# Optimization experiments

Hardware: AMD Instinct MI355X
Metric: run time of the kernel (lower is better)

Reference implementation:

```python
import jax, jax.numpy as jnp
import numpy as np

B, N, D = 4, 2048, 512
H, DH = 8, 64
MLP = 2048
EPS = 1e-5


def setup_inputs() -> dict:
    key = jax.random.key(0)
    ks = jax.random.split(key, 8)
    s = lambda fan_in: 1.0 / np.sqrt(fan_in)
    return {
        "x": jax.random.normal(ks[0], (B, N, D), jnp.float32),
        "ln1_g": jnp.ones((D,), jnp.float32),
        "ln1_b": jnp.zeros((D,), jnp.float32),
        "Wqkv": jax.random.normal(ks[1], (D, 3 * H * DH), jnp.float32) * s(D),
        "temperature": jnp.asarray(np.log(DH ** -0.5), jnp.float32),
        "Wo": jax.random.normal(ks[2], (H * DH, D), jnp.float32) * s(H * DH),
        "bo": jnp.zeros((D,), jnp.float32),
        "ln2_g": jnp.ones((D,), jnp.float32),
        "ln2_b": jnp.zeros((D,), jnp.float32),
        "W1": jax.random.normal(ks[3], (D, MLP), jnp.float32) * s(D),
        "b1": jnp.zeros((MLP,), jnp.float32),
        "W2": jax.random.normal(ks[4], (MLP, D), jnp.float32) * s(MLP),
        "b2": jnp.zeros((D,), jnp.float32),
    }


def _layernorm(x, g, b):
    mu = jnp.mean(x, axis=-1, keepdims=True)
    var = jnp.var(x, axis=-1, keepdims=True)
    return (x - mu) * jax.lax.rsqrt(var + EPS) * g + b


def _lsa(x, Wqkv, temperature, Wo, bo):
    b, n, _ = x.shape
    qkv = x @ Wqkv  # [b, n, 3*H*DH]
    q, k, v = jnp.split(qkv, 3, axis=-1)
    rs = lambda t: t.reshape(b, n, H, DH).transpose(0, 2, 1, 3)  # b h n d
    q, k, v = rs(q), rs(k), rs(v)
    dots = jnp.einsum("bhnd,bhmd->bhnm", q, k) * jnp.exp(temperature)
    mask_value = -jnp.finfo(dots.dtype).max
    eye = jnp.eye(n, dtype=bool)
    dots = jnp.where(eye, mask_value, dots)  # mask diagonal (LSA)
    attn = jax.nn.softmax(dots, axis=-1)
    out = jnp.einsum("bhnm,bhmd->bhnd", attn, v)
    out = out.transpose(0, 2, 1, 3).reshape(b, n, H * DH)
    return out @ Wo + bo


def _ffn(x, W1, b1, W2, b2):
    h = jax.nn.gelu(x @ W1 + b1, approximate=False)
    return h @ W2 + b2


def reference(x, ln1_g, ln1_b, Wqkv, temperature, Wo, bo,
              ln2_g, ln2_b, W1, b1, W2, b2):
    y = _lsa(_layernorm(x, ln1_g, ln1_b), Wqkv, temperature, Wo, bo) + x
    z = _ffn(_layernorm(y, ln2_g, ln2_b), W1, b1, W2, b2) + y
    return (z, x)
```

## Files before the change

kernel.cpp:

```cpp
#include <hip/hip_runtime.h>
#include <math.h>

typedef __attribute__((ext_vector_type(4))) float f32x4;
typedef __attribute__((ext_vector_type(8))) short short8;

#define DEV __device__ __forceinline__

DEV short f2bf(float f){
  union { float f; unsigned u; } v; v.f = f;
  unsigned r = v.u + 0x7fffu + ((v.u >> 16) & 1u);
  return (short)(r >> 16);
}
DEV float bf2f(short s){
  union { unsigned u; float f; } v; v.u = ((unsigned)(unsigned short)s) << 16; return v.f;
}
DEV float exp2_hw(float x){ float r; asm("v_exp_f32 %0, %1" : "=v"(r) : "v"(x)); return r; }
DEV float rcp_hw(float x){ float r; asm("v_rcp_f32 %0, %1" : "=v"(r) : "v"(x)); return r; }
DEV unsigned cvtpk(float a, float b){
  unsigned r; asm("v_cvt_pk_bf16_f32 %0, %1, %2" : "=v"(r) : "v"(a), "v"(b)); return r;
}
DEV void gload_lds16(const short* src, short* lds){
  __builtin_amdgcn_global_load_lds(
      (const __attribute__((address_space(1))) void*)src,
      (__attribute__((address_space(3))) void*)lds, 16, 0, 0);
}
DEV float gelu_fast(float v){
  float u = v * (0.79788456f + 0.03567741f * v * v);
  float e = exp2_hw(u * 2.88539008f);
  float th = 1.0f - 2.0f * rcp_hw(e + 1.0f);
  return 0.5f * v * (1.0f + th);
}

__global__ __launch_bounds__(256) void transpose_all_kernel(
    const float* __restrict__ Wqkv, short* __restrict__ wqkv_t,
    const float* __restrict__ Wo,   short* __restrict__ wo_t,
    const float* __restrict__ W1,   short* __restrict__ w1_t,
    const float* __restrict__ W2,   short* __restrict__ w2_t)
{
  int bid = blockIdx.x;
  const float* W; short* Wt; int K, N, nbx, local;
  if (bid < 768)       { W = Wqkv; Wt = wqkv_t; K = 512;  N = 1536; nbx = 48; local = bid; }
  else if (bid < 1024) { W = Wo;   Wt = wo_t;   K = 512;  N = 512;  nbx = 16; local = bid - 768; }
  else if (bid < 2048) { W = W1;   Wt = w1_t;   K = 512;  N = 2048; nbx = 64; local = bid - 1024; }
  else                 { W = W2;   Wt = w2_t;   K = 2048; N = 512;  nbx = 16; local = bid - 2048; }
  __shared__ float tile[32][33];
  int nb = (local % nbx) * 32, kb = (local / nbx) * 32;
  int tx = threadIdx.x & 31, ty = threadIdx.x >> 5;
  #pragma unroll
  for (int i = ty; i < 32; i += 8)
    tile[i][tx] = W[(size_t)(kb + i) * N + nb + tx];
  __syncthreads();
  #pragma unroll
  for (int i = ty; i < 32; i += 8)
    Wt[(size_t)(nb + i) * K + kb + tx] = f2bf(tile[tx][i]);
}

template<int COPYX>
__global__ __launch_bounds__(256) void ln_kernel(
    const float* __restrict__ x, const float* __restrict__ g,
    const float* __restrict__ b, short* __restrict__ out,
    float* __restrict__ xcopy)
{
  int row  = blockIdx.x * 4 + (threadIdx.x >> 6);
  int lane = threadIdx.x & 63;
  const float* xr = x + (size_t)row * 512 + lane * 8;
  f32x4 v0 = *(const f32x4*)(xr);
  f32x4 v1 = *(const f32x4*)(xr + 4);
  float s  = (v0[0]+v0[1]+v0[2]+v0[3]) + (v1[0]+v1[1]+v1[2]+v1[3]);
  float sq = (v0[0]*v0[0]+v0[1]*v0[1]+v0[2]*v0[2]+v0[3]*v0[3])
           + (v1[0]*v1[0]+v1[1]*v1[1]+v1[2]*v1[2]+v1[3]*v1[3]);
  #pragma unroll
  for (int off = 1; off < 64; off <<= 1) {
    s  += __shfl_xor(s, off);
    sq += __shfl_xor(sq, off);
  }
  float mu  = s * (1.0f / 512.0f);
  float var = sq * (1.0f / 512.0f) - mu * mu;
  float rstd = rsqrtf(var + 1e-5f);
  f32x4 g0 = *(const f32x4*)(g + lane * 8);
  f32x4 g1 = *(const f32x4*)(g + lane * 8 + 4);
  f32x4 b0 = *(const f32x4*)(b + lane * 8);
  f32x4 b1 = *(const f32x4*)(b + lane * 8 + 4);
  float o[8];
  #pragma unroll
  for (int j = 0; j < 4; ++j) o[j]     = (v0[j] - mu) * rstd * g0[j] + b0[j];
  #pragma unroll
  for (int j = 0; j < 4; ++j) o[4 + j] = (v1[j] - mu) * rstd * g1[j] + b1[j];
  uint4 pk;
  pk.x = cvtpk(o[0], o[1]); pk.y = cvtpk(o[2], o[3]);
  pk.z = cvtpk(o[4], o[5]); pk.w = cvtpk(o[6], o[7]);
  *(uint4*)(out + (size_t)row * 512 + lane * 8) = pk;
  if (COPYX) {
    float* xc = xcopy + (size_t)row * 512 + lane * 8;
    *(f32x4*)(xc)     = v0;
    *(f32x4*)(xc + 4) = v1;
  }
}

__global__ __launch_bounds__(256) void ln_bf_kernel(
    const short* __restrict__ x, const float* __restrict__ g,
    const float* __restrict__ b, short* __restrict__ out)
{
  int row  = blockIdx.x * 4 + (threadIdx.x >> 6);
  int lane = threadIdx.x & 63;
  short8 raw = *(const short8*)(x + (size_t)row * 512 + lane * 8);
  float v[8];
  #pragma unroll
  for (int j = 0; j < 8; ++j) v[j] = bf2f(raw[j]);
  float s = 0.f, sq = 0.f;
  #pragma unroll
  for (int j = 0; j < 8; ++j) { s += v[j]; sq += v[j] * v[j]; }
  #pragma unroll
  for (int off = 1; off < 64; off <<= 1) {
    s  += __shfl_xor(s, off);
    sq += __shfl_xor(sq, off);
  }
  float mu  = s * (1.0f / 512.0f);
  float var = sq * (1.0f / 512.0f) - mu * mu;
  float rstd = rsqrtf(var + 1e-5f);
  f32x4 g0 = *(const f32x4*)(g + lane * 8);
  f32x4 g1 = *(const f32x4*)(g + lane * 8 + 4);
  f32x4 b0 = *(const f32x4*)(b + lane * 8);
  f32x4 b1 = *(const f32x4*)(b + lane * 8 + 4);
  float o[8];
  #pragma unroll
  for (int j = 0; j < 4; ++j) o[j]     = (v[j] - mu) * rstd * g0[j] + b0[j];
  #pragma unroll
  for (int j = 0; j < 4; ++j) o[4 + j] = (v[4+j] - mu) * rstd * g1[j] + b1[j];
  uint4 pk;
  pk.x = cvtpk(o[0], o[1]); pk.y = cvtpk(o[2], o[3]);
  pk.z = cvtpk(o[4], o[5]); pk.w = cvtpk(o[6], o[7]);
  *(uint4*)(out + (size_t)row * 512 + lane * 8) = pk;
}

template<int EPI, int BM, typename OutT>
__global__ __launch_bounds__(256) void gemm_bt_kernel(
    const short* __restrict__ A, const short* __restrict__ Bt,
    OutT* __restrict__ C, const float* __restrict__ bias,
    const float* __restrict__ resid, const short* __restrict__ residb,
    int M, int N, int K)
{
  constexpr int MFR = BM / 32;
  constexpr int NFR = 4;
  constexpr int AI  = BM / 64;
  constexpr int BUF = BM * 32 + 128 * 32;
  __shared__ __align__(16) short smem[3 * BUF];

  int tid = threadIdx.x;
  int lane = tid & 63, wid = tid >> 6;
  int l16 = lane & 15, lq = lane >> 4;

  int gx = gridDim.x;
  int nwg = gx * gridDim.y;
  int orig = blockIdx.y * gx + blockIdx.x;
  int swz = (orig & 7) * (nwg >> 3) + (orig >> 3);
  int bn = swz % gx, bm = swz / gx;

  int wm = wid >> 1, wn = wid & 1;

  const short* gaP[AI];
  const short* gbP[2];
  #pragma unroll
  for (int i = 0; i < AI; ++i) {
    int gg = i * 4 + wid;
    gaP[i] = A + (size_t)(bm * BM + gg * 16 + l16) * K + lq * 8;
  }
  #pragma unroll
  for (int i = 0; i < 2; ++i) {
    int gg = i * 4 + wid;
    gbP[i] = Bt + (size_t)(bn * 128 + gg * 16 + l16) * K + lq * 8;
  }

  auto STAGE = [&](int bufi, int k0) {
    short* base = smem + bufi * BUF;
    #pragma unroll
    for (int i = 0; i < AI; ++i)
      gload_lds16(gaP[i] + k0, base + (i * 4 + wid) * 512);
    #pragma unroll
    for (int i = 0; i < 2; ++i)
      gload_lds16(gbP[i] + k0, base + BM * 32 + (i * 4 + wid) * 512);
  };

  f32x4 acc[MFR][NFR] = {};

  STAGE(0, 0);
  STAGE(1, 32);

  int nt = K >> 5;
  for (int t = 0; t < nt; ++t) {
    if (t + 1 < nt) {
      if constexpr (AI == 2) asm volatile("s_waitcnt vmcnt(4)" ::: "memory");
      else                   asm volatile("s_waitcnt vmcnt(3)" ::: "memory");
    } else {
      asm volatile("s_waitcnt vmcnt(0)" ::: "memory");
    }
    __builtin_amdgcn_s_barrier();
    __builtin_amdgcn_sched_barrier(0);
    if (t + 2 < nt) STAGE((t + 2) % 3, (t + 2) << 5);

    const short* base = smem + (t % 3) * BUF;
    short8 af[MFR], bfr[NFR];
    #pragma unroll
    for (int m = 0; m < MFR; ++m)
      af[m] = *(const short8*)(base + (wm * MFR + m) * 512 + lane * 8);
    #pragma unroll
    for (int n = 0; n < NFR; ++n)
      bfr[n] = *(const short8*)(base + BM * 32 + (wn * NFR + n) * 512 + lane * 8);
    __builtin_amdgcn_s_setprio(1);
    #pragma unroll
    for (int m = 0; m < MFR; ++m)
      #pragma unroll
      for (int n = 0; n < NFR; ++n)
        acc[m][n] = __builtin_amdgcn_mfma_f32_16x16x32_bf16(af[m], bfr[n], acc[m][n], 0, 0, 0);
    __builtin_amdgcn_s_setprio(0);
  }

  float bv[NFR];
  #pragma unroll
  for (int n = 0; n < NFR; ++n)
    bv[n] = bias[bn * 128 + (wn * NFR + n) * 16 + l16];

  #pragma unroll
  for (int m = 0; m < MFR; ++m) {
    #pragma unroll
    for (int r = 0; r < 4; ++r) {
      int row = bm * BM + (wm * MFR + m) * 16 + lq * 4 + r;
      #pragma unroll
      for (int n = 0; n < NFR; ++n) {
        int col = bn * 128 + (wn * NFR + n) * 16 + l16;
        float v = acc[m][n][r] + bv[n];
        if (EPI == 4) v += resid[(size_t)row * N + col];
        if (EPI == 5) v += bf2f(residb[(size_t)row * N + col]);
        if constexpr (sizeof(OutT) == 2)
          ((short*)C)[(size_t)row * N + col] = f2bf(v);
        else
          ((float*)C)[(size_t)row * N + col] = v;
      }
    }
  }
}

template<int EPI>
__global__ __launch_bounds__(512) void gemm256_kernel(
    const short* __restrict__ A, const short* __restrict__ Bt,
    short* __restrict__ C, const float* __restrict__ bias,
    short* __restrict__ vt, int M, int N, int K)
{
  constexpr int BUF = 24576;
  __shared__ __align__(16) short smem[3 * BUF];

  int tid = threadIdx.x;
  int lane = tid & 63, wid = tid >> 6;
  int l16 = lane & 15, lq = lane >> 4;

  int gx = gridDim.x;
  int nwg = gx * gridDim.y;
  int orig = blockIdx.y * gx + blockIdx.x;
  int swz = (orig & 7) * (nwg >> 3) + (orig >> 3);
  int bn = swz % gx, bm = swz / gx;

  int wm = wid >> 1, wn = wid & 1;

  const short* gaP[4];
  const short* gbP[2];
  #pragma unroll
  for (int i = 0; i < 4; ++i) {
    int g = i * 8 + wid;
    gaP[i] = A + (size_t)(bm * 256 + (g >> 1) * 16 + l16) * K + (g & 1) * 32 + lq * 8;
  }
  #pragma unroll
  for (int i = 0; i < 2; ++i) {
    int g = i * 8 + wid;
    gbP[i] = Bt + (size_t)(bn * 128 + (g >> 1) * 16 + l16) * K + (g & 1) * 32 + lq * 8;
  }

  auto STAGE = [&](int bufi, int k0) {
    short* base = smem + bufi * BUF;
    #pragma unroll
    for (int i = 0; i < 4; ++i)
      gload_lds16(gaP[i] + k0, base + (i * 8 + wid) * 512);
    #pragma unroll
    for (int i = 0; i < 2; ++i)
      gload_lds16(gbP[i] + k0, base + 16384 + (i * 8 + wid) * 512);
  };

  f32x4 acc[4][4] = {};

  STAGE(0, 0);
  STAGE(1, 64);

  int nt = K >> 6;
  for (int t = 0; t < nt; ++t) {
    if (t + 1 < nt) asm volatile("s_waitcnt vmcnt(6)" ::: "memory");
    else            asm volatile("s_waitcnt vmcnt(0)" ::: "memory");
    __builtin_amdgcn_s_barrier();
    __builtin_amdgcn_sched_barrier(0);
    if (t + 2 < nt) STAGE((t + 2) % 3, (t + 2) << 6);

    const short* base = smem + (t % 3) * BUF;
    #pragma unroll
    for (int kc = 0; kc < 2; ++kc) {
      short8 af[4], bfr[4];
      #pragma unroll
      for (int m = 0; m < 4; ++m)
        af[m] = *(const short8*)(base + ((wm * 4 + m) * 2 + kc) * 512 + lane * 8);
      #pragma unroll
      for (int n = 0; n < 4; ++n)
        bfr[n] = *(const short8*)(base + 16384 + ((wn * 4 + n) * 2 + kc) * 512 + lane * 8);
      __builtin_amdgcn_s_setprio(1);
      #pragma unroll
      for (int m = 0; m < 4; ++m)
        #pragma unroll
        for (int n = 0; n < 4; ++n)
          acc[m][n] = __builtin_amdgcn_mfma_f32_16x16x32_bf16(af[m], bfr[n], acc[m][n], 0, 0, 0);
      __builtin_amdgcn_s_setprio(0);
    }
  }

  if (EPI == 3 && bn >= 8) {
    __syncthreads();
    short* T = smem;
    #pragma unroll
    for (int m = 0; m < 4; ++m)
      #pragma unroll
      for (int n = 0; n < 4; ++n) {
        int c = wn * 64 + n * 16 + l16;
        #pragma unroll
        for (int r = 0; r < 4; ++r) {
          int rowl = wm * 64 + m * 16 + lq * 4 + r;
          T[c * 256 + (rowl ^ ((c & 7) << 4))] = f2bf(acc[m][n][r]);
        }
      }
    __syncthreads();
    int b2 = bm >> 3;
    int nnb = (bm & 7) * 256;
    int tn = tid & 31, cw = tid >> 5;
    #pragma unroll
    for (int c8 = 0; c8 < 8; ++c8) {
      int c = c8 * 16 + cw;
      short8 v = *(const short8*)(T + c * 256 + ((tn * 8) ^ ((c & 7) << 4)));
      if (tn & 1) {
        short8 w;
        #pragma unroll
        for (int j = 0; j < 8; ++j) w[j] = v[j ^ 4];
        v = w;
      }
      int c2 = bn * 128 + c - 1024;
      int bh = b2 * 8 + (c2 >> 6);
      int d  = c2 & 63;
      *(short8*)(vt + ((size_t)(bh * 64 + d)) * 2048 + nnb + tn * 8) = v;
    }
    return;
  }

  #pragma unroll
  for (int m = 0; m < 4; ++m) {
    #pragma unroll
    for (int r = 0; r < 4; ++r) {
      int row = bm * 256 + (wm * 4 + m) * 16 + lq * 4 + r;
      #pragma unroll
      for (int n = 0; n < 4; ++n) {
        int col = bn * 128 + (wn * 4 + n) * 16 + l16;
        C[(size_t)row * N + col] = f2bf(acc[m][n][r]);
      }
    }
  }
}

__global__ __launch_bounds__(512, 2) void gemm8p_kernel(
    const short* __restrict__ A, const short* __restrict__ Bt,
    short* __restrict__ C, const float* __restrict__ bias,
    int M, int N, int K)
{
  __shared__ __align__(16) short smem[2 * 32768];

  int tid = threadIdx.x;
  int lane = tid & 63, wid = tid >> 6;
  int l16 = lane & 15, lq = lane >> 4;
  int wm = wid >> 2, wn = wid & 3;

  int gx = gridDim.x;
  int nwg = gx * gridDim.y;
  int orig = blockIdx.y * gx + blockIdx.x;
  int swz = (orig & 7) * (nwg >> 3) + (orig >> 3);
  int bn = swz % gx, bm = swz / gx;

  const short* gaP[4];
  const short* gbP[4];
  #pragma unroll
  for (int i = 0; i < 4; ++i) {
    int idx = i * 512 + tid;
    int g = idx >> 6, ln = idx & 63;
    gaP[i] = A  + (size_t)(bm * 256 + (g >> 1) * 16 + (ln & 15)) * K
                + (g & 1) * 32 + (ln >> 4) * 8;
    gbP[i] = Bt + (size_t)(bn * 256 + (g >> 1) * 16 + (ln & 15)) * K
                + (g & 1) * 32 + (ln >> 4) * 8;
  }

  auto STAGE_A = [&](int buf, int k0) {
    short* dst = smem + buf * 32768;
    #pragma unroll
    for (int i = 0; i < 4; ++i)
      gload_lds16(gaP[i] + k0, dst + ((size_t)(i * 512 + tid)) * 8);
  };
  auto STAGE_B_LO = [&](int buf, int k0) {
    short* dst = smem + buf * 32768 + 16384;
    #pragma unroll
    for (int i = 0; i < 2; ++i)
      gload_lds16(gbP[i] + k0, dst + ((size_t)(i * 512 + tid)) * 8);
  };
  auto STAGE_B_HI = [&](int buf, int k0) {
    short* dst = smem + buf * 32768 + 16384;
    #pragma unroll
    for (int i = 2; i < 4; ++i)
      gload_lds16(gbP[i] + k0, dst + ((size_t)(i * 512 + tid)) * 8);
  };

  f32x4 acc[8][4] = {};

  STAGE_A(0, 0);
  STAGE_B_LO(0, 0); STAGE_B_HI(0, 0);
  STAGE_B_LO(1, 64); STAGE_B_HI(1, 64);
  asm volatile("s_waitcnt vmcnt(4)" ::: "memory");
  __builtin_amdgcn_s_barrier();

  int nt = K >> 6;
  for (int t = 0; t < nt; ++t) {
    int cur = t & 1;
    const short* As_ = smem + cur * 32768;
    const short* Bs_ = As_ + 16384;
    short8 bf[4][2];

    #pragma unroll
    for (int p = 0; p < 4; ++p) {
      short8 af[2][2];
      #pragma unroll
      for (int mm = 0; mm < 2; ++mm)
        #pragma unroll
        for (int kc = 0; kc < 2; ++kc)
          af[mm][kc] = *(const short8*)(As_ + ((wm * 8 + 2 * p + mm) * 2 + kc) * 512 + lane * 8);
      if (p == 0) {
        #pragma unroll
        for (int n = 0; n < 4; ++n)
          #pragma unroll
          for (int kc = 0; kc < 2; ++kc)
            bf[n][kc] = *(const short8*)(Bs_ + ((wn * 4 + n) * 2 + kc) * 512 + lane * 8);
      }
      if (p == 0 && t + 1 < nt) STAGE_A(cur ^ 1, (t + 1) << 6);
      if (p == 1 && t + 2 < nt) STAGE_B_LO(cur, (t + 2) << 6);
      if (p == 2 && t + 2 < nt) STAGE_B_HI(cur, (t + 2) << 6);

      __builtin_amdgcn_s_barrier();
      asm volatile("s_waitcnt lgkmcnt(0)" ::: "memory");
      __builtin_amdgcn_sched_barrier(0);
      __builtin_amdgcn_s_setprio(1);
      #pragma unroll
      for (int mm = 0; mm < 2; ++mm)
        #pragma unroll
        for (int n = 0; n < 4; ++n)
          #pragma unroll
          for (int kc = 0; kc < 2; ++kc)
            acc[2 * p + mm][n] = __builtin_amdgcn_mfma_f32_16x16x32_bf16(
                af[mm][kc], bf[n][kc], acc[2 * p + mm][n], 0, 0, 0);
      __builtin_amdgcn_s_setprio(0);
      if (p < 3) {
        __builtin_amdgcn_s_barrier();
      } else {
        if (t + 2 < nt) asm volatile("s_waitcnt vmcnt(4)" ::: "memory");
        else            asm volatile("s_waitcnt vmcnt(0)" ::: "memory");
        __builtin_amdgcn_s_barrier();
      }
    }
  }

  float bv[4];
  #pragma unroll
  for (int n = 0; n < 4; ++n)
    bv[n] = bias[bn * 256 + (wn * 4 + n) * 16 + l16];
  #pragma unroll
  for (int m = 0; m < 8; ++m) {
    #pragma unroll
    for (int r = 0; r < 4; ++r) {
      int row = bm * 256 + wm * 128 + m * 16 + lq * 4 + r;
      #pragma unroll
      for (int n = 0; n < 4; ++n) {
        int col = bn * 256 + (wn * 4 + n) * 16 + l16;
        C[(size_t)row * N + col] = f2bf(gelu_fast(acc[m][n][r] + bv[n]));
      }
    }
  }
}

__global__ __launch_bounds__(512, 4) void attn_kernel(
    const short* __restrict__ qkv, const short* __restrict__ vt,
    const float* __restrict__ temp_ptr,
    short* __restrict__ Op0, short* __restrict__ Op1, float* __restrict__ Lbuf)
{
  __shared__ __align__(16) short smem[16384];

  int tid = threadIdx.x;
  int lane = tid & 63, wid = tid >> 6;
  int l16 = lane & 15, lq = lane >> 4;
  int hi = lq >> 1, lq0 = lq & 1;

  int orig = blockIdx.y * 8 + blockIdx.x;
  int swz = (orig & 7) * 64 + (orig >> 3);
  int qb = swz & 7;
  int rr = swz >> 3;
  int bh = rr & 31, slice = rr >> 5;
  int b = bh >> 3, h = bh & 7;

  const short* qbase = qkv + (size_t)b * 2048 * 1536 + h * 64;
  const short* kbase = qbase + 512;
  const short* vbase = vt + (size_t)bh * 64 * 2048;
  int kslice = slice * 1024;

  float scale = __expf(temp_ptr[0]) * 1.44269504f;
  int q0 = qb * 256 + wid * 32;

  short8 qfrag[2][2];
  #pragma unroll
  for (int qf = 0; qf < 2; ++qf) {
    int qrow = q0 + qf * 16 + l16;
    #pragma unroll
    for (int c = 0; c < 2; ++c) {
      short8 raw = *(const short8*)(qbase + (size_t)qrow * 1536 + c * 32 + lq * 8);
      short8 sc;
      #pragma unroll
      for (int j = 0; j < 8; ++j) sc[j] = f2bf(bf2f(raw[j]) * scale);
      qfrag[qf][c] = sc;
    }
  }

  f32x4 accO[2][4] = {};
  float l[2] = {0.f, 0.f};

  auto STAGE = [&](int bufi, int k0) {
    int sub = wid >> 1, cc = wid & 1;
    const short* srcK = kbase + (size_t)(k0 + sub * 16 + l16) * 1536 + cc * 32 + lq * 8;
    gload_lds16(srcK, smem + bufi * 4096 + wid * 512);
    const short* srcV = vbase + (size_t)(sub * 16 + l16) * 2048 + k0 + cc * 32 + lq * 8;
    gload_lds16(srcV, smem + 8192 + bufi * 4096 + wid * 512);
  };

  STAGE(0, kslice);
  asm volatile("s_waitcnt vmcnt(0)");
  __syncthreads();

  for (int t = 0; t < 16; ++t) {
    int cur = t & 1;
    int k0 = kslice + t * 64;
    if (t + 1 < 16) STAGE(cur ^ 1, k0 + 64);

    const short* kls = smem + cur * 4096;
    const short* vls = smem + 8192 + cur * 4096;

    f32x4 accS[2][4] = {};
    #pragma unroll
    for (int s = 0; s < 4; ++s) {
      short8 kf0 = *(const short8*)(kls + (s * 2 + 0) * 512 + lane * 8);
      short8 kf1 = *(const short8*)(kls + (s * 2 + 1) * 512 + lane * 8);
      #pragma unroll
      for (int qf = 0; qf < 2; ++qf) {
        accS[qf][s] = __builtin_amdgcn_mfma_f32_16x16x32_bf16(kf0, qfrag[qf][0], accS[qf][s], 0, 0, 0);
        accS[qf][s] = __builtin_amdgcn_mfma_f32_16x16x32_bf16(kf1, qfrag[qf][1], accS[qf][s], 0, 0, 0);
      }
    }

    if ((q0 & ~63) == k0) {
      #pragma unroll
      for (int qf = 0; qf < 2; ++qf) {
        int qg = q0 + qf * 16 + l16;
        #pragma unroll
        for (int s = 0; s < 4; ++s)
          #pragma unroll
          for (int r = 0; r < 4; ++r)
            if (k0 + s * 16 + lq * 4 + r == qg) accS[qf][s][r] = -30000.f;
      }
    }

    short8 pa[2][2];
    #pragma unroll
    for (int qf = 0; qf < 2; ++qf) {
      float sum = 0.f;
      unsigned W[4][2];
      #pragma unroll
      for (int s = 0; s < 4; ++s) {
        float p0 = exp2_hw(accS[qf][s][0]);
        float p1 = exp2_hw(accS[qf][s][1]);
        float p2 = exp2_hw(accS[qf][s][2]);
        float p3 = exp2_hw(accS[qf][s][3]);
        sum += (p0 + p1) + (p2 + p3);
        W[s][0] = cvtpk(p0, p1);
        W[s][1] = cvtpk(p2, p3);
      }
      sum += __shfl_xor(sum, 16);
      sum += __shfl_xor(sum, 32);
      l[qf] += sum;

      unsigned K0[2], S0[2], K2[2], S2[2], R0[2], R2[2];
      #pragma unroll
      for (int w = 0; w < 2; ++w) {
        K0[w] = hi ? W[1][w] : W[0][w];
        S0[w] = hi ? W[0][w] : W[1][w];
        K2[w] = hi ? W[3][w] : W[2][w];
        S2[w] = hi ? W[2][w] : W[3][w];
      }
      #pragma unroll
      for (int w = 0; w < 2; ++w) {
        R0[w] = (unsigned)__shfl_xor((int)S0[w], 32);
        R2[w] = (unsigned)__shfl_xor((int)S2[w], 32);
      }
      bool sw = (hi != lq0);
      unsigned FA[2], FB[2], sA[2], sB[2], GA[2], GB[2];
      #pragma unroll
      for (int w = 0; w < 2; ++w) {
        sA[w] = sw ? K0[w] : R0[w];  FA[w] = sw ? R0[w] : K0[w];
        sB[w] = sw ? K2[w] : R2[w];  FB[w] = sw ? R2[w] : K2[w];
      }
      #pragma unroll
      for (int w = 0; w < 2; ++w) {
        GA[w] = (unsigned)__shfl_xor((int)sA[w], 16);
        GB[w] = (unsigned)__shfl_xor((int)sB[w], 16);
      }
      union { unsigned u[4]; short8 s8; } p0u, p1u;
      p0u.u[0] = FA[0]; p0u.u[1] = FA[1]; p0u.u[2] = GA[0]; p0u.u[3] = GA[1];
      p1u.u[0] = FB[0]; p1u.u[1] = FB[1]; p1u.u[2] = GB[0]; p1u.u[3] = GB[1];
      pa[qf][0] = p0u.s8;
      pa[qf][1] = p1u.s8;
    }

    short8 vfr[4][2];
    #pragma unroll
    for (int d = 0; d < 4; ++d) {
      vfr[d][0] = *(const short8*)(vls + (d * 2 + 0) * 512 + lane * 8);
      vfr[d][1] = *(const short8*)(vls + (d * 2 + 1) * 512 + lane * 8);
    }
    #pragma unroll
    for (int qf = 0; qf < 2; ++qf)
      #pragma unroll
      for (int d = 0; d < 4; ++d) {
        accO[qf][d] = __builtin_amdgcn_mfma_f32_16x16x32_bf16(vfr[d][0], pa[qf][0], accO[qf][d], 0, 0, 0);
        accO[qf][d] = __builtin_amdgcn_mfma_f32_16x16x32_bf16(vfr[d][1], pa[qf][1], accO[qf][d], 0, 0, 0);
      }

    __syncthreads();
  }

  short* op = slice ? Op1 : Op0;
  #pragma unroll
  for (int qf = 0; qf < 2; ++qf) {
    int qg = q0 + qf * 16 + l16;
    if (lq == 0) Lbuf[(size_t)(slice * 32 + bh) * 2048 + qg] = l[qf];
    size_t rowoff = (size_t)(b * 2048 + qg) * 512 + h * 64;
    #pragma unroll
    for (int d = 0; d < 4; ++d) {
      unsigned w0 = cvtpk(accO[qf][d][0], accO[qf][d][1]);
      unsigned w1 = cvtpk(accO[qf][d][2], accO[qf][d][3]);
      uint2 pk; pk.x = w0; pk.y = w1;
      *(uint2*)(op + rowoff + d * 16 + lq * 4) = pk;
    }
  }
}

__global__ __launch_bounds__(256) void attn_combine_kernel(
    const short* __restrict__ Op0, const short* __restrict__ Op1,
    const float* __restrict__ Lbuf, short* __restrict__ out)
{
  int idx = blockIdx.x * 256 + threadIdx.x;
  size_t e = (size_t)idx * 8;
  int row = (int)(e >> 9);
  int col = (int)(e & 511);
  int b = row >> 11, q = row & 2047;
  int bh = b * 8 + (col >> 6);
  float l0 = Lbuf[(size_t)bh * 2048 + q];
  float l1 = Lbuf[(size_t)(32 + bh) * 2048 + q];
  float inv = rcp_hw(l0 + l1);
  short8 a = *(const short8*)(Op0 + e);
  short8 c = *(const short8*)(Op1 + e);
  float o[8];
  #pragma unroll
  for (int j = 0; j < 8; ++j) o[j] = (bf2f(a[j]) + bf2f(c[j])) * inv;
  uint4 pk;
  pk.x = cvtpk(o[0], o[1]); pk.y = cvtpk(o[2], o[3]);
  pk.z = cvtpk(o[4], o[5]); pk.w = cvtpk(o[6], o[7]);
  *(uint4*)(out + e) = pk;
}

extern "C" void kernel_launch(void* const* d_in, const int* in_sizes, int n_in,
                              void* d_out, int out_size, void* d_ws, size_t ws_size,
                              hipStream_t stream)
{
  const float* x    = (const float*)d_in[0];
  const float* ln1g = (const float*)d_in[1];
  const float* ln1b = (const float*)d_in[2];
  const float* Wqkv = (const float*)d_in[3];
  const float* temp = (const float*)d_in[4];
  const float* Wo   = (const float*)d_in[5];
  const float* bo   = (const float*)d_in[6];
  const float* ln2g = (const float*)d_in[7];
  const float* ln2b = (const float*)d_in[8];
  const float* W1   = (const float*)d_in[9];
  const float* b1   = (const float*)d_in[10];
  const float* W2   = (const float*)d_in[11];
  const float* b2   = (const float*)d_in[12];
  float* out = (float*)d_out;

  char* ws = (char*)d_ws;
  short* wqkv_t = (short*)(ws);
  float* lpart  = (float*)(ws);
  short* wo_t   = (short*)(ws + 1572864);
  short* w1_t   = (short*)(ws + 2097152);
  short* w2_t   = (short*)(ws + 4194304);
  short* h      = (short*)(ws + 6291456);
  short* qkv    = (short*)(ws + 14680064);
  short* attn   = (short*)(ws + 39845888);
  short* ybf    = (short*)(ws + 48234496);
  short* vt     = (short*)(ws + 48234496);
  short* t      = (short*)(ws + 14680064);

  const int M = 8192;

  transpose_all_kernel<<<3072, 256, 0, stream>>>(
      Wqkv, wqkv_t, Wo, wo_t, W1, w1_t, W2, w2_t);

  ln_kernel<1><<<M / 4, 256, 0, stream>>>(x, ln1g, ln1b, h, out + (size_t)M * 512);

  gemm256_kernel<3><<<dim3(1536 / 128, M / 256), 512, 0, stream>>>(
      h, wqkv_t, qkv, nullptr, vt, M, 1536, 512);

  attn_kernel<<<dim3(8, 64), 512, 0, stream>>>(qkv, vt, temp, attn, h, lpart);
  attn_combine_kernel<<<M * 512 / 8 / 256, 256, 0, stream>>>(attn, h, lpart, attn);

  gemm_bt_kernel<4, 64, short><<<dim3(512 / 128, M / 64), 256, 0, stream>>>(
      attn, wo_t, ybf, bo, x, nullptr, M, 512, 512);

  ln_bf_kernel<<<M / 4, 256, 0, stream>>>(ybf, ln2g, ln2b, h);

  gemm8p_kernel<<<dim3(2048 / 256, M / 256), 512, 0, stream>>>(
      h, w1_t, t, b1, M, 2048, 512);

  gemm_bt_kernel<5, 64, float><<<dim3(512 / 128, M / 64), 256, 0, stream>>>(
      t, w2_t, out, b2, nullptr, ybf, M, 512, 2048);
}
```

Before: 195.1 us.

## Merge weight transpose with LN1 and deepen gemm_bt K-tile to 64

Fuses the weight transpose/bf16 cast kernel and the first layernorm into a single prep launch, removing one kernel launch and letting the two independent workloads run concurrently. Separately doubles the K-step of the small-N GEMM kernel (used for Wo and W2 projections) from 32 to 64, doubling staged LDS buffers and issuing two MFMA sub-steps per barrier, which halves barrier/wait overhead per unit of work. The larger LDS footprint (3 buffers of (BM+128)*64 shorts) may reduce occupancy.

```diff
diff --git a/kernel.cpp b/kernel.cpp
--- a/kernel.cpp
+++ b/kernel.cpp
@@ -31,37 +31,35 @@
   return 0.5f * v * (1.0f + th);
 }
 
-__global__ __launch_bounds__(256) void transpose_all_kernel(
+__global__ __launch_bounds__(256) void prep_kernel(
     const float* __restrict__ Wqkv, short* __restrict__ wqkv_t,
     const float* __restrict__ Wo,   short* __restrict__ wo_t,
     const float* __restrict__ W1,   short* __restrict__ w1_t,
-    const float* __restrict__ W2,   short* __restrict__ w2_t)
+    const float* __restrict__ W2,   short* __restrict__ w2_t,
+    const float* __restrict__ x, const float* __restrict__ ln1g,
+    const float* __restrict__ ln1b, short* __restrict__ h,
+    float* __restrict__ xcopy)
 {
   int bid = blockIdx.x;
-  const float* W; short* Wt; int K, N, nbx, local;
-  if (bid < 768)       { W = Wqkv; Wt = wqkv_t; K = 512;  N = 1536; nbx = 48; local = bid; }
-  else if (bid < 1024) { W = Wo;   Wt = wo_t;   K = 512;  N = 512;  nbx = 16; local = bid - 768; }
-  else if (bid < 2048) { W = W1;   Wt = w1_t;   K = 512;  N = 2048; nbx = 64; local = bid - 1024; }
-  else                 { W = W2;   Wt = w2_t;   K = 2048; N = 512;  nbx = 16; local = bid - 2048; }
-  __shared__ float tile[32][33];
-  int nb = (local % nbx) * 32, kb = (local / nbx) * 32;
-  int tx = threadIdx.x & 31, ty = threadIdx.x >> 5;
-  #pragma unroll
-  for (int i = ty; i < 32; i += 8)
-    tile[i][tx] = W[(size_t)(kb + i) * N + nb + tx];
-  __syncthreads();
-  #pragma unroll
-  for (int i = ty; i < 32; i += 8)
-    Wt[(size_t)(nb + i) * K + kb + tx] = f2bf(tile[tx][i]);
-}
-
-template<int COPYX>
-__global__ __launch_bounds__(256) void ln_kernel(
-    const float* __restrict__ x, const float* __restrict__ g,
-    const float* __restrict__ b, short* __restrict__ out,
-    float* __restrict__ xcopy)
-{
-  int row  = blockIdx.x * 4 + (threadIdx.x >> 6);
+  if (bid < 3072) {
+    const float* W; short* Wt; int K, N, nbx, local;
+    if (bid < 768)       { W = Wqkv; Wt = wqkv_t; K = 512;  N = 1536; nbx = 48; local = bid; }
+    else if (bid < 1024) { W = Wo;   Wt = wo_t;   K = 512;  N = 512;  nbx = 16; local = bid - 768; }
+    else if (bid < 2048) { W = W1;   Wt = w1_t;   K = 512;  N = 2048; nbx = 64; local = bid - 1024; }
+    else                 { W = W2;   Wt = w2_t;   K = 2048; N = 512;  nbx = 16; local = bid - 2048; }
+    __shared__ float tile[32][33];
+    int nb = (local % nbx) * 32, kb = (local / nbx) * 32;
+    int tx = threadIdx.x & 31, ty = threadIdx.x >> 5;
+    #pragma unroll
+    for (int i = ty; i < 32; i += 8)
+      tile[i][tx] = W[(size_t)(kb + i) * N + nb + tx];
+    __syncthreads();
+    #pragma unroll
+    for (int i = ty; i < 32; i += 8)
+      Wt[(size_t)(nb + i) * K + kb + tx] = f2bf(tile[tx][i]);
+    return;
+  }
+  int row  = (bid - 3072) * 4 + (threadIdx.x >> 6);
   int lane = threadIdx.x & 63;
   const float* xr = x + (size_t)row * 512 + lane * 8;
   f32x4 v0 = *(const f32x4*)(xr);
@@ -77,10 +75,10 @@
   float mu  = s * (1.0f / 512.0f);
   float var = sq * (1.0f / 512.0f) - mu * mu;
   float rstd = rsqrtf(var + 1e-5f);
-  f32x4 g0 = *(const f32x4*)(g + lane * 8);
-  f32x4 g1 = *(const f32x4*)(g + lane * 8 + 4);
-  f32x4 b0 = *(const f32x4*)(b + lane * 8);
-  f32x4 b1 = *(const f32x4*)(b + lane * 8 + 4);
+  f32x4 g0 = *(const f32x4*)(ln1g + lane * 8);
+  f32x4 g1 = *(const f32x4*)(ln1g + lane * 8 + 4);
+  f32x4 b0 = *(const f32x4*)(ln1b + lane * 8);
+  f32x4 b1 = *(const f32x4*)(ln1b + lane * 8 + 4);
   float o[8];
   #pragma unroll
   for (int j = 0; j < 4; ++j) o[j]     = (v0[j] - mu) * rstd * g0[j] + b0[j];
@@ -89,12 +87,10 @@
   uint4 pk;
   pk.x = cvtpk(o[0], o[1]); pk.y = cvtpk(o[2], o[3]);
   pk.z = cvtpk(o[4], o[5]); pk.w = cvtpk(o[6], o[7]);
-  *(uint4*)(out + (size_t)row * 512 + lane * 8) = pk;
-  if (COPYX) {
-    float* xc = xcopy + (size_t)row * 512 + lane * 8;
-    *(f32x4*)(xc)     = v0;
-    *(f32x4*)(xc + 4) = v1;
-  }
+  *(uint4*)(h + (size_t)row * 512 + lane * 8) = pk;
+  float* xc = xcopy + (size_t)row * 512 + lane * 8;
+  *(f32x4*)(xc)     = v0;
+  *(f32x4*)(xc + 4) = v1;
 }
 
 __global__ __launch_bounds__(256) void ln_bf_kernel(
@@ -142,8 +138,8 @@
 {
   constexpr int MFR = BM / 32;
   constexpr int NFR = 4;
-  constexpr int AI  = BM / 64;
-  constexpr int BUF = BM * 32 + 128 * 32;
+  constexpr int AI  = BM / 32;
+  constexpr int BUF = (BM + 128) * 64;
   __shared__ __align__(16) short smem[3 * BUF];
 
   int tid = threadIdx.x;
@@ -159,16 +155,16 @@
   int wm = wid >> 1, wn = wid & 1;
 
   const short* gaP[AI];
-  const short* gbP[2];
+  const short* gbP[4];
   #pragma unroll
   for (int i = 0; i < AI; ++i) {
-    int gg = i * 4 + wid;
-    gaP[i] = A + (size_t)(bm * BM + gg * 16 + l16) * K + lq * 8;
-  }
-  #pragma unroll
-  for (int i = 0; i < 2; ++i) {
-    int gg = i * 4 + wid;
-    gbP[i] = Bt + (size_t)(bn * 128 + gg * 16 + l16) * K + lq * 8;
+    int g = i * 4 + wid;
+    gaP[i] = A + (size_t)(bm * BM + (g >> 1) * 16 + l16) * K + (g & 1) * 32 + lq * 8;
+  }
+  #pragma unroll
+  for (int i = 0; i < 4; ++i) {
+    int g = i * 4 + wid;
+    gbP[i] = Bt + (size_t)(bn * 128 + (g >> 1) * 16 + l16) * K + (g & 1) * 32 + lq * 8;
   }
 
   auto STAGE = [&](int bufi, int k0) {
@@ -177,42 +173,41 @@
     for (int i = 0; i < AI; ++i)
       gload_lds16(gaP[i] + k0, base + (i * 4 + wid) * 512);
     #pragma unroll
-    for (int i = 0; i < 2; ++i)
-      gload_lds16(gbP[i] + k0, base + BM * 32 + (i * 4 + wid) * 512);
+    for (int i = 0; i < 4; ++i)
+      gload_lds16(gbP[i] + k0, base + BM * 64 + (i * 4 + wid) * 512);
   };
 
   f32x4 acc[MFR][NFR] = {};
 
   STAGE(0, 0);
-  STAGE(1, 32);
-
-  int nt = K >> 5;
+  STAGE(1, 64);
+
+  int nt = K >> 6;
   for (int t = 0; t < nt; ++t) {
-    if (t + 1 < nt) {
-      if constexpr (AI == 2) asm volatile("s_waitcnt vmcnt(4)" ::: "memory");
-      else                   asm volatile("s_waitcnt vmcnt(3)" ::: "memory");
-    } else {
-      asm volatile("s_waitcnt vmcnt(0)" ::: "memory");
-    }
+    if (t + 1 < nt) asm volatile("s_waitcnt vmcnt(6)" ::: "memory");
+    else            asm volatile("s_waitcnt vmcnt(0)" ::: "memory");
     __builtin_amdgcn_s_barrier();
     __builtin_amdgcn_sched_barrier(0);
-    if (t + 2 < nt) STAGE((t + 2) % 3, (t + 2) << 5);
+    if (t + 2 < nt) STAGE((t + 2) % 3, (t + 2) << 6);
 
     const short* base = smem + (t % 3) * BUF;
-    short8 af[MFR], bfr[NFR];
-    #pragma unroll
-    for (int m = 0; m < MFR; ++m)
-      af[m] = *(const short8*)(base + (wm * MFR + m) * 512 + lane * 8);
-    #pragma unroll
-    for (int n = 0; n < NFR; ++n)
-      bfr[n] = *(const short8*)(base + BM * 32 + (wn * NFR + n) * 512 + lane * 8);
-    __builtin_amdgcn_s_setprio(1);
-    #pragma unroll
-    for (int m = 0; m < MFR; ++m)
+    #pragma unroll
+    for (int kc = 0; kc < 2; ++kc) {
+      short8 af[MFR], bfr[NFR];
+      #pragma unroll
+      for (int m = 0; m < MFR; ++m)
+        af[m] = *(const short8*)(base + ((wm * MFR + m) * 2 + kc) * 512 + lane * 8);
       #pragma unroll
       for (int n = 0; n < NFR; ++n)
-        acc[m][n] = __builtin_amdgcn_mfma_f32_16x16x32_bf16(af[m], bfr[n], acc[m][n], 0, 0, 0);
-    __builtin_amdgcn_s_setprio(0);
+        bfr[n] = *(const short8*)(base + BM * 64 + ((wn * NFR + n) * 2 + kc) * 512 + lane * 8);
+      __builtin_amdgcn_s_setprio(1);
+      #pragma unroll
+      for (int m = 0; m < MFR; ++m)
+        #pragma unroll
+        for (int n = 0; n < NFR; ++n)
+          acc[m][n] = __builtin_amdgcn_mfma_f32_16x16x32_bf16(af[m], bfr[n], acc[m][n], 0, 0, 0);
+      __builtin_amdgcn_s_setprio(0);
+    }
   }
 
   float bv[NFR];
@@ -721,10 +716,9 @@
 
   const int M = 8192;
 
-  transpose_all_kernel<<<3072, 256, 0, stream>>>(
-      Wqkv, wqkv_t, Wo, wo_t, W1, w1_t, W2, w2_t);
-
-  ln_kernel<1><<<M / 4, 256, 0, stream>>>(x, ln1g, ln1b, h, out + (size_t)M * 512);
+  prep_kernel<<<3072 + 2048, 256, 0, stream>>>(
+      Wqkv, wqkv_t, Wo, wo_t, W1, w1_t, W2, w2_t,
+      x, ln1g, ln1b, h, out + (size_t)M * 512);
 
   gemm256_kernel<3><<<dim3(1536 / 128, M / 256), 512, 0, stream>>>(
       h, wqkv_t, qkv, nullptr, vt, M, 1536, 512);
```

After: 191.8 us. Within noise of the previous version (-1.7%).
